# Kernel optimization log

Hardware: AMD Instinct MI355X
Metric: run time of the kernel (lower is better)

The kernel has to match this reference:

```python
import jax, jax.numpy as jnp
import numpy as np

B, N, D = 16, 1369, 1024
HID, NH = 512, 8
SCALE = np.sqrt(D // NH)


def _pos_encoding_2d(n, d):
    ps = int(np.sqrt(n))  # 37; n is a perfect square here
    div = jnp.exp(jnp.arange(0, d // 2, 2, dtype=jnp.float32) * (-np.log(10000.0) / (d // 2)))
    rows = (jnp.arange(n) // ps).astype(jnp.float32)
    cols = (jnp.arange(n) % ps).astype(jnp.float32)
    def interleave(s, c):
        return jnp.stack([s, c], axis=-1).reshape(n, -1)
    half_row = interleave(jnp.sin(rows[:, None] * div), jnp.cos(rows[:, None] * div))
    half_col = interleave(jnp.sin(cols[:, None] * div), jnp.cos(cols[:, None] * div))
    return jnp.concatenate([half_row, half_col], axis=-1)  # [n, d]


def _center_bias(n, strength=0.3):
    ps = int(np.sqrt(n))
    c = ps // 2
    y, x = jnp.meshgrid(jnp.arange(ps, dtype=jnp.float32), jnp.arange(ps, dtype=jnp.float32), indexing='ij')
    d2 = (x - c) ** 2 + (y - c) ** 2
    sigma = ps / 6.0
    return (jnp.exp(-d2 / (2.0 * sigma ** 2)).reshape(-1)) * strength  # [n]


def setup_inputs() -> dict:
    key = jax.random.key(0)
    ks = jax.random.split(key, 16)
    s = 0.02
    return {
        'patch_tokens': jax.random.normal(ks[0], (B, N, D), dtype=jnp.float32),
        'curiosity_score': jax.random.uniform(ks[1], (B,), dtype=jnp.float32),
        'Wq': jax.random.normal(ks[2], (D, D), dtype=jnp.float32) * s,
        'bq': jax.random.uniform(ks[3], (D,), minval=-0.05, maxval=0.05, dtype=jnp.float32),
        'Wk': jax.random.normal(ks[4], (D, D), dtype=jnp.float32) * s,
        'bk': jax.random.uniform(ks[5], (D,), minval=-0.05, maxval=0.05, dtype=jnp.float32),
        'Wv': jax.random.normal(ks[6], (D, D), dtype=jnp.float32) * s,
        'bv': jnp.zeros((D,), dtype=jnp.float32),
        'Wc1': jax.random.normal(ks[7], (1, HID // 8), dtype=jnp.float32) * s,
        'bc1': jnp.zeros((HID // 8,), dtype=jnp.float32),
        'Wc2': jax.random.normal(ks[8], (HID // 8, NH), dtype=jnp.float32) * s,
        'bc2': jnp.zeros((NH,), dtype=jnp.float32),
        'Wp1': jax.random.normal(ks[9], (D, HID), dtype=jnp.float32) * s,
        'bp1': jnp.zeros((HID,), dtype=jnp.float32),
        'Wp2': jax.random.normal(ks[10], (HID, HID // 4), dtype=jnp.float32) * s,
        'bp2': jnp.zeros((HID // 4,), dtype=jnp.float32),
        'adaptive_weight': jnp.float32(0.5),
    }


def reference(patch_tokens, curiosity_score, Wq, bq, Wk, bk, Wv, bv,
              Wc1, bc1, Wc2, bc2, Wp1, bp1, Wp2, bp2, adaptive_weight):
    b, n, d = patch_tokens.shape
    x = patch_tokens + _pos_encoding_2d(n, d)[None]  # [B,N,D]

    q = x @ Wq + bq
    k = x @ Wk + bk
    v = x @ Wv + bv

    scores = jnp.einsum('bqd,bkd->bqk', q, k) / SCALE          # [B,N,N]
    attn = jax.nn.softmax(scores, axis=-1)                     # dropout p=0 / eval
    attended = jnp.einsum('bqk,bkd->bqd', attn, v)             # [B,N,D]

    cb = _center_bias(n)[None]                                 # [1,N]
    VAR_EPS = 1e-6

    pa = attn.mean(axis=1) + cb
    # fallback chain (data-dependent in torch; expressed with jnp.where)
    pa2 = jnp.diagonal(attn, axis1=-2, axis2=-1) + cb
    pa = jnp.where(jnp.var(pa, ddof=1) < VAR_EPS, pa2, pa)
    pa3 = attn.max(axis=-1) + cb
    pa = jnp.where(jnp.var(pa, ddof=1) < VAR_EPS, pa3, pa)
    norms = jnp.linalg.norm(x, axis=-1)
    noise = jax.random.normal(jax.random.key(42), norms.shape, dtype=norms.dtype) * 0.1 * jnp.std(norms, ddof=1)
    pa = jnp.where(jnp.var(pa, ddof=1) < VAR_EPS, norms + noise, pa)

    pa = pa / (pa.sum(axis=-1, keepdims=True) + 1e-8)

    # curiosity modulation
    h = jax.nn.relu(curiosity_score[:, None] @ Wc1 + bc1)
    cm = jax.nn.sigmoid(h @ Wc2 + bc2)                         # [B,NH]
    cw = cm.mean(axis=-1, keepdims=True)                       # [B,1]
    modulated = pa * (1.0 + cw)
    fa = adaptive_weight * modulated + (1.0 - adaptive_weight) * pa

    fa = jnp.clip(fa, 1e-8, None)
    fa = fa / (fa.sum(axis=-1, keepdims=True) + 1e-8)

    weighted = jnp.sum(attended * fa[..., None], axis=1)       # [B,D]
    focal = jax.nn.relu(weighted @ Wp1 + bp1) @ Wp2 + bp2      # [B,HID//4]
    return focal, fa
```

## Files before the change

kernel.cpp:

```cpp
#include <hip/hip_runtime.h>
#include <hip/hip_bf16.h>
#include <cstdint>

#define B_   16
#define N_   1369
#define NP   1536
#define D_   1024
#define NQKV 3072

typedef __bf16 bf16x8_t __attribute__((ext_vector_type(8)));
typedef __bf16 bf16x4_t __attribute__((ext_vector_type(4)));
typedef float  f32x4_t  __attribute__((ext_vector_type(4)));

__device__ __forceinline__ float  bf2f(__bf16 x) { return (float)x; }
__device__ __forceinline__ __bf16 f2bf(float x)  { return (__bf16)x; }

#define GLOAD_LDS16(g, l) __builtin_amdgcn_global_load_lds( \
    (const __attribute__((address_space(1))) void*)(g),     \
    (__attribute__((address_space(3))) void*)(l), 16, 0, 0)

__global__ __launch_bounds__(256)
void pos_kernel(float* __restrict__ pos)
{
    const int idx = blockIdx.x * 256 + threadIdx.x;
    if (idx >= N_ * D_) return;
    const int n = idx >> 10, f = idx & 1023;
    const int row = n / 37, col = n - row * 37;
    const float base = (f < 512) ? (float)row : (float)col;
    const int  t2   = (f & 511) >> 1;
    const float dv  = __expf(-0.03597789207803197f * (float)t2);
    const float ang = base * dv;
    pos[idx] = (f & 1) ? cosf(ang) : sinf(ang);
}

__global__ __launch_bounds__(256)
void addpos_kernel(const float* __restrict__ patch, const float* __restrict__ pos,
                   __bf16* __restrict__ X)
{
    const long tid = (long)blockIdx.x * 256 + threadIdx.x;
    const long e   = tid * 4;
    const int  f   = (int)(e & 1023);
    const long nb  = e >> 10;
    const int  n   = (int)(nb % NP);
    const long b   = nb / NP;
    bf16x4_t o;
    if (n < N_) {
        const float4 p = *(const float4*)(patch + ((b * N_ + n) << 10) + f);
        const float4 q = *(const float4*)(pos + ((long)n << 10) + f);
        o[0] = f2bf(p.x + q.x); o[1] = f2bf(p.y + q.y);
        o[2] = f2bf(p.z + q.z); o[3] = f2bf(p.w + q.w);
    } else {
        o[0] = o[1] = o[2] = o[3] = f2bf(0.f);
    }
    *(bf16x4_t*)(X + e) = o;
}

__global__ __launch_bounds__(256)
void wcast_kernel(const float* __restrict__ W0, const float* __restrict__ W1,
                  const float* __restrict__ W2,
                  __bf16* __restrict__ T0, __bf16* __restrict__ T1, __bf16* __restrict__ T2)
{
    const float* W = blockIdx.z == 0 ? W0 : (blockIdx.z == 1 ? W1 : W2);
    __bf16*      T = blockIdx.z == 0 ? T0 : (blockIdx.z == 1 ? T1 : T2);
    __shared__ float tile[64][65];
    const int o0 = blockIdx.x * 64, i0 = blockIdx.y * 64;
    const int t = threadIdx.x;
    const int tr = t >> 4, tc = (t & 15) * 4;
    #pragma unroll
    for (int rr = 0; rr < 64; rr += 16) {
        float4 v = *(const float4*)(W + (long)(i0 + rr + tr) * 1024 + o0 + tc);
        tile[rr + tr][tc + 0] = v.x; tile[rr + tr][tc + 1] = v.y;
        tile[rr + tr][tc + 2] = v.z; tile[rr + tr][tc + 3] = v.w;
    }
    __syncthreads();
    #pragma unroll
    for (int rr = 0; rr < 64; rr += 16) {
        bf16x4_t o;
        o[0] = f2bf(tile[tc + 0][rr + tr]); o[1] = f2bf(tile[tc + 1][rr + tr]);
        o[2] = f2bf(tile[tc + 2][rr + tr]); o[3] = f2bf(tile[tc + 3][rr + tr]);
        *(bf16x4_t*)(T + (long)(o0 + rr + tr) * 1024 + i0 + tc) = o;
    }
}

__global__ __launch_bounds__(256)
void bcat_kernel(const float* __restrict__ bq, const float* __restrict__ bk,
                 const float* __restrict__ bv, float* __restrict__ bcat)
{
    const int i = blockIdx.x * 256 + threadIdx.x;
    if (i >= NQKV) return;
    const int p = i >> 10, j = i & 1023;
    bcat[i] = p == 0 ? bq[j] : (p == 1 ? bk[j] : bv[j]);
}

template<int HAS_BIAS>
__global__ __launch_bounds__(512, 2)
void gemm256(const __bf16* __restrict__ A, const __bf16* __restrict__ Bt,
             __bf16* __restrict__ C, const float* __restrict__ bias,
             int lda, int ldb, int ldc, int Kd, float scale,
             long sA, long sB, long sC, int tilesN, int tilesPerBatch, int cpx)
{
    __shared__ __bf16 lds[65536];
    const int bid = blockIdx.x;
    const int vt  = (bid & 7) * cpx + (bid >> 3);
    const int bz  = vt / tilesPerBatch;
    const int rem = vt - bz * tilesPerBatch;
    const int ty  = rem / tilesN;
    const int tx  = rem - ty * tilesN;
    A  += (long)bz * sA;  Bt += (long)bz * sB;  C += (long)bz * sC;
    const int m0 = ty * 256, n0 = tx * 256;

    const int t  = threadIdx.x;
    const int w  = t >> 6, l = t & 63;
    const int wr = w >> 2, wc = w & 3;
    const int lr = l & 15, lh = l >> 4;

    const int laneF  = (lr * 64 + ((lh * 16) ^ (((lr >> 3) & 1) << 5))) >> 1;
    const int rstage = w * 16 + (l >> 2);
    const int kstage = ((l & 3) * 8) ^ (((l >> 5) & 1) << 4);

    const __bf16* Ag = A  + (long)(m0 + rstage) * lda + kstage;
    const __bf16* Bg = Bt + (long)(n0 + rstage) * ldb + kstage;
    __bf16* dA = lds + (w * 2) * 512;
    __bf16* dB = lds + 16384 + (w * 2) * 512;

#define SA_(buf, half, kt) do {                                       \
    const __bf16* g_ = Ag + (long)(half) * 128 * lda + (kt) * 64;     \
    __bf16* d_ = dA + (buf) * 32768 + (half) * 8192;                  \
    GLOAD_LDS16(g_, d_); GLOAD_LDS16(g_ + 32, d_ + 512); } while (0)
#define SB_(buf, half, kt) do {                                       \
    const __bf16* g_ = Bg + (long)(half) * 128 * ldb + (kt) * 64;     \
    __bf16* d_ = dB + (buf) * 32768 + (half) * 8192;                  \
    GLOAD_LDS16(g_, d_); GLOAD_LDS16(g_ + 32, d_ + 512); } while (0)

    f32x4_t acc[8][4] = {};
    bf16x8_t bfr[4][2];

#define BREADS_() do { const __bf16* bp_ = lds + cbB + laneF;                              \
    bfr[0][0] = *(const bf16x8_t*)(bp_);        bfr[0][1] = *(const bf16x8_t*)(bp_ + 512); \
    bfr[1][0] = *(const bf16x8_t*)(bp_ + 1024); bfr[1][1] = *(const bf16x8_t*)(bp_ + 1536);\
    bfr[2][0] = *(const bf16x8_t*)(bp_ + 2048); bfr[2][1] = *(const bf16x8_t*)(bp_ + 2560);\
    bfr[3][0] = *(const bf16x8_t*)(bp_ + 3072); bfr[3][1] = *(const bf16x8_t*)(bp_ + 3584);} while (0)

#define PHASE_(p, P0R, STG, VMW) do {                                                  \
    const __bf16* ap_ = lds + cbase + wr * 8192 + (p) * 2048 + laneF;                  \
    bf16x8_t a00 = *(const bf16x8_t*)(ap_);                                            \
    bf16x8_t a01 = *(const bf16x8_t*)(ap_ + 512);                                      \
    bf16x8_t a10 = *(const bf16x8_t*)(ap_ + 1024);                                     \
    bf16x8_t a11 = *(const bf16x8_t*)(ap_ + 1536);                                     \
    P0R;                                                                               \
    STG;                                                                               \
    __builtin_amdgcn_s_barrier();                                                      \
    asm volatile("s_waitcnt lgkmcnt(0)" ::: "memory");                                 \
    __builtin_amdgcn_sched_barrier(0);                                                 \
    __builtin_amdgcn_s_setprio(1);                                                     \
    _Pragma("unroll") for (int nn = 0; nn < 4; ++nn)                                   \
      acc[(p)*2+0][nn] = __builtin_amdgcn_mfma_f32_16x16x32_bf16(a00, bfr[nn][0], acc[(p)*2+0][nn], 0, 0, 0); \
    _Pragma("unroll") for (int nn = 0; nn < 4; ++nn)                                   \
      acc[(p)*2+1][nn] = __builtin_amdgcn_mfma_f32_16x16x32_bf16(a10, bfr[nn][0], acc[(p)*2+1][nn], 0, 0, 0); \
    _Pragma("unroll") for (int nn = 0; nn < 4; ++nn)                                   \
      acc[(p)*2+0][nn] = __builtin_amdgcn_mfma_f32_16x16x32_bf16(a01, bfr[nn][1], acc[(p)*2+0][nn], 0, 0, 0); \
    _Pragma("unroll") for (int nn = 0; nn < 4; ++nn)                                   \
      acc[(p)*2+1][nn] = __builtin_amdgcn_mfma_f32_16x16x32_bf16(a11, bfr[nn][1], acc[(p)*2+1][nn], 0, 0, 0); \
    __builtin_amdgcn_s_setprio(0);                                                     \
    VMW;                                                                               \
    __builtin_amdgcn_s_barrier();                                                      \
  } while (0)

    const int NT = Kd >> 6;
    SA_(0, 0, 0); SA_(0, 1, 0); SB_(0, 0, 0); SB_(0, 1, 0);
    SB_(1, 0, 1); SB_(1, 1, 1);
    asm volatile("s_waitcnt vmcnt(4)" ::: "memory");
    __builtin_amdgcn_s_barrier();

    for (int tk = 0; tk < NT; ++tk) {
        const int c  = tk & 1, o = c ^ 1;
        const int t1 = (tk + 1 < NT) ? tk + 1 : NT - 1;
        const int t2 = (tk + 2 < NT) ? tk + 2 : NT - 1;
        const int cbase = c * 32768;
        const int cbB   = cbase + 16384 + wc * 4096;
        PHASE_(0, BREADS_(), SA_(o, 0, t1), ((void)0));
        PHASE_(1, ((void)0), SA_(o, 1, t1), ((void)0));
        PHASE_(2, ((void)0), SB_(c, 0, t2), ((void)0));
        PHASE_(3, ((void)0), SB_(c, 1, t2),
               asm volatile("s_waitcnt vmcnt(4)" ::: "memory"));
    }

    #pragma unroll
    for (int mi = 0; mi < 8; ++mi) {
        const int row = m0 + wr * 128 + mi * 16 + lh * 4;
        #pragma unroll
        for (int nn = 0; nn < 4; ++nn) {
            const int col = n0 + wc * 64 + nn * 16 + lr;
            const float bb = HAS_BIAS ? bias[col] : 0.0f;
            #pragma unroll
            for (int q = 0; q < 4; ++q)
                C[(long)(row + q) * ldc + col] = f2bf(acc[mi][nn][q] * scale + bb);
        }
    }
#undef SA_
#undef SB_
#undef BREADS_
#undef PHASE_
}

__global__ __launch_bounds__(256)
void softmax_kernel(__bf16* __restrict__ S)
{
    const int q = blockIdx.x, b = blockIdx.y;
    __bf16* row = S + ((long)b * NP + q) * NP;
    const int t = threadIdx.x;
    float v[6];
    float m = -1e30f;
    #pragma unroll
    for (int i = 0; i < 6; ++i) {
        const int k = t + i * 256;
        float x = -1e30f;
        if (k < N_) x = bf2f(row[k]);
        v[i] = x;
        m = fmaxf(m, x);
    }
    __shared__ float red[8];
    #pragma unroll
    for (int o = 32; o; o >>= 1) m = fmaxf(m, __shfl_xor(m, o));
    if (!(t & 63)) red[t >> 6] = m;
    __syncthreads();
    m = fmaxf(fmaxf(red[0], red[1]), fmaxf(red[2], red[3]));
    float s = 0.f;
    #pragma unroll
    for (int i = 0; i < 6; ++i) {
        const int k = t + i * 256;
        if (k < N_) { const float e = __expf(v[i] - m); v[i] = e; s += e; }
    }
    #pragma unroll
    for (int o = 32; o; o >>= 1) s += __shfl_xor(s, o);
    if (!(t & 63)) red[4 + (t >> 6)] = s;
    __syncthreads();
    s = red[4] + red[5] + red[6] + red[7];
    const float inv = 1.f / s;
    #pragma unroll
    for (int i = 0; i < 6; ++i) {
        const int k = t + i * 256;
        if (k < N_)      row[k] = f2bf(v[i] * inv);
        else             row[k] = f2bf(0.f);
    }
}

template<int WEIGHTED>
__global__ __launch_bounds__(256)
void colsum_kernel(const __bf16* __restrict__ attn, const float* __restrict__ wv,
                   float* __restrict__ out)
{
    const int k = blockIdx.x * 256 + threadIdx.x;
    const int b = blockIdx.y;
    const int q0 = blockIdx.z * 172;
    const int q1 = (q0 + 172 < N_) ? q0 + 172 : N_;
    if (k >= N_) return;
    const __bf16* base = attn + (long)b * NP * NP + k;
    float s = 0.f;
    for (int q = q0; q < q1; ++q) {
        float a = bf2f(base[(long)q * NP]);
        if (WEIGHTED) a *= wv[b * NP + q];
        s += a;
    }
    atomicAdd(out + b * NP + k, s);
}

__global__ __launch_bounds__(256)
void fa_kernel(const float* __restrict__ pa_raw, const float* __restrict__ curiosity,
               const float* __restrict__ Wc1, const float* __restrict__ bc1,
               const float* __restrict__ Wc2, const float* __restrict__ bc2,
               const float* __restrict__ aw_p,
               float* __restrict__ fa_ws, float* __restrict__ out_fa)
{
    const int b = blockIdx.x, t = threadIdx.x;
    __shared__ float hsh[64];
    __shared__ float red[8];
    __shared__ float cwsh;
    if (t < 64) hsh[t] = fmaxf(0.f, curiosity[b] * Wc1[t] + bc1[t]);
    __syncthreads();
    if (t < 8) {
        float a = bc2[t];
        for (int j = 0; j < 64; ++j) a += hsh[j] * Wc2[j * 8 + t];
        red[t] = 1.f / (1.f + __expf(-a));
    }
    __syncthreads();
    if (t == 0) {
        float cw = 0.f;
        for (int i = 0; i < 8; ++i) cw += red[i];
        cwsh = cw * 0.125f;
    }
    __syncthreads();
    const float aw   = aw_p[0];
    const float modf = 1.f + aw * cwsh;
    const float sig  = 37.f / 6.f;
    const float inv2s2 = 1.f / (2.f * sig * sig);
    float pv[6];
    float s1 = 0.f;
    #pragma unroll
    for (int i = 0; i < 6; ++i) {
        const int k = t + i * 256;
        float p = 0.f;
        if (k < N_) {
            const int y = k / 37, x = k - y * 37;
            const float d2 = (float)((x - 18) * (x - 18) + (y - 18) * (y - 18));
            const float cb = 0.3f * __expf(-d2 * inv2s2);
            p = pa_raw[b * NP + k] * (1.f / 1369.f) + cb;
        }
        pv[i] = p; s1 += p;
    }
    #pragma unroll
    for (int o = 32; o; o >>= 1) s1 += __shfl_xor(s1, o);
    __syncthreads();
    if (!(t & 63)) red[t >> 6] = s1;
    __syncthreads();
    s1 = red[0] + red[1] + red[2] + red[3];
    const float inv1 = 1.f / (s1 + 1e-8f);
    float s2 = 0.f;
    #pragma unroll
    for (int i = 0; i < 6; ++i) {
        const int k = t + i * 256;
        if (k < N_) {
            const float f = fmaxf(pv[i] * inv1 * modf, 1e-8f);
            pv[i] = f; s2 += f;
        }
    }
    #pragma unroll
    for (int o = 32; o; o >>= 1) s2 += __shfl_xor(s2, o);
    if (!(t & 63)) red[4 + (t >> 6)] = s2;
    __syncthreads();
    s2 = red[4] + red[5] + red[6] + red[7];
    const float inv2 = 1.f / (s2 + 1e-8f);
    #pragma unroll
    for (int i = 0; i < 6; ++i) {
        const int k = t + i * 256;
        if (k < N_) {
            const float f = pv[i] * inv2;
            fa_ws[b * NP + k]  = f;
            out_fa[b * N_ + k] = f;
        }
    }
}

__global__ __launch_bounds__(256)
void weighted_kernel(const float* __restrict__ g, const __bf16* __restrict__ V,
                     int ldv, float* __restrict__ wout)
{
    const int b  = blockIdx.y;
    const int k0 = blockIdx.x * 86;
    const int k1 = (k0 + 86 < N_) ? k0 + 86 : N_;
    const int d  = threadIdx.x * 4;
    float a0 = 0, a1 = 0, a2 = 0, a3 = 0;
    const __bf16* vb = V + (long)b * NP * ldv + d;
    for (int k = k0; k < k1; ++k) {
        const float gv = g[b * NP + k];
        bf16x4_t vv = *(const bf16x4_t*)(vb + (long)k * ldv);
        a0 += gv * bf2f(vv[0]); a1 += gv * bf2f(vv[1]);
        a2 += gv * bf2f(vv[2]); a3 += gv * bf2f(vv[3]);
    }
    atomicAdd(wout + b * D_ + d + 0, a0);
    atomicAdd(wout + b * D_ + d + 1, a1);
    atomicAdd(wout + b * D_ + d + 2, a2);
    atomicAdd(wout + b * D_ + d + 3, a3);
}

__global__ __launch_bounds__(256)
void focal_kernel(const float* __restrict__ weighted, const float* __restrict__ Wp1,
                  const float* __restrict__ bp1, const float* __restrict__ Wp2,
                  const float* __restrict__ bp2, float* __restrict__ out)
{
    const int b = blockIdx.x, t = threadIdx.x;
    __shared__ float wsh[1024];
    __shared__ float hsh[512];
    for (int i = t; i < 1024; i += 256) wsh[i] = weighted[b * 1024 + i];
    __syncthreads();
    for (int j = t; j < 512; j += 256) {
        float a = bp1[j];
        for (int d2 = 0; d2 < 1024; ++d2) a += wsh[d2] * Wp1[d2 * 512 + j];
        hsh[j] = fmaxf(a, 0.f);
    }
    __syncthreads();
    for (int o = t; o < 128; o += 256) {
        float a = bp2[o];
        for (int j = 0; j < 512; ++j) a += hsh[j] * Wp2[j * 128 + o];
        out[b * 128 + o] = a;
    }
}

extern "C" void kernel_launch(void* const* d_in, const int* in_sizes, int n_in,
                              void* d_out, int out_size, void* d_ws, size_t ws_size,
                              hipStream_t stream)
{
    const float* patch     = (const float*)d_in[0];
    const float* curiosity = (const float*)d_in[1];
    const float* Wq  = (const float*)d_in[2];
    const float* bq  = (const float*)d_in[3];
    const float* Wk  = (const float*)d_in[4];
    const float* bk  = (const float*)d_in[5];
    const float* Wv  = (const float*)d_in[6];
    const float* bv  = (const float*)d_in[7];
    const float* Wc1 = (const float*)d_in[8];
    const float* bc1 = (const float*)d_in[9];
    const float* Wc2 = (const float*)d_in[10];
    const float* bc2 = (const float*)d_in[11];
    const float* Wp1 = (const float*)d_in[12];
    const float* bp1 = (const float*)d_in[13];
    const float* Wp2 = (const float*)d_in[14];
    const float* bp2 = (const float*)d_in[15];
    const float* aw  = (const float*)d_in[16];
    float* out = (float*)d_out;

    char* ws = (char*)d_ws;
    size_t off = 0;
    auto alloc = [&](size_t bytes) -> char* {
        char* p = ws + off;
        off += (bytes + 255) & ~(size_t)255;
        return p;
    };
    float*  pos  = (float*) alloc((size_t)N_ * D_ * 4);
    __bf16* X    = (__bf16*)alloc((size_t)B_ * NP * D_ * 2);
    __bf16* WT   = (__bf16*)alloc((size_t)3 * D_ * D_ * 2);
    const size_t S_BYTES = (size_t)B_ * NP * NP * 2;
    if (off < S_BYTES) off = S_BYTES;
    __bf16* S    = (__bf16*)ws;
    __bf16* QKV  = (__bf16*)alloc((size_t)B_ * NP * NQKV * 2);
    float*  pa   = (float*) alloc((size_t)B_ * NP * 4);
    float*  faw  = (float*) alloc((size_t)B_ * NP * 4);
    float*  gbuf = (float*) alloc((size_t)B_ * NP * 4);
    float*  wsum = (float*) alloc((size_t)B_ * D_ * 4);
    float*  bcat = (float*) alloc((size_t)NQKV * 4);

    (void)hipMemsetAsync(pa,   0, (size_t)B_ * NP * 4, stream);
    (void)hipMemsetAsync(gbuf, 0, (size_t)B_ * NP * 4, stream);
    (void)hipMemsetAsync(wsum, 0, (size_t)B_ * D_ * 4, stream);

    pos_kernel<<<(N_ * D_ + 255) / 256, 256, 0, stream>>>(pos);
    addpos_kernel<<<(int)((size_t)B_ * NP * D_ / 4 / 256), 256, 0, stream>>>(patch, pos, X);
    {
        dim3 g(16, 16, 3);
        wcast_kernel<<<g, 256, 0, stream>>>(Wq, Wk, Wv,
                                            WT, WT + D_ * D_, WT + 2 * D_ * D_);
    }
    bcat_kernel<<<(NQKV + 255) / 256, 256, 0, stream>>>(bq, bk, bv, bcat);
    {
        const int nwg = 96 * 12;
        gemm256<1><<<nwg, 512, 0, stream>>>(X, WT, QKV, bcat,
                                            D_, D_, NQKV, D_, 1.0f,
                                            0, 0, 0, 12, nwg, nwg / 8);
    }
    {
        const int nwg = 36 * B_;
        gemm256<0><<<nwg, 512, 0, stream>>>(QKV, QKV + D_, S, nullptr,
                                            NQKV, NQKV, NP, D_,
                                            0.08838834764831845f,
                                            (long)NP * NQKV, (long)NP * NQKV,
                                            (long)NP * NP, 6, 36, nwg / 8);
    }
    {
        dim3 g(N_, B_);
        softmax_kernel<<<g, 256, 0, stream>>>(S);
    }
    {
        dim3 g(6, B_, 8);
        colsum_kernel<0><<<g, 256, 0, stream>>>(S, nullptr, pa);
    }
    fa_kernel<<<B_, 256, 0, stream>>>(pa, curiosity, Wc1, bc1, Wc2, bc2, aw,
                                      faw, out + B_ * 128);
    {
        dim3 g(6, B_, 8);
        colsum_kernel<1><<<g, 256, 0, stream>>>(S, faw, gbuf);
    }
    {
        dim3 g(16, B_);
        weighted_kernel<<<g, 256, 0, stream>>>(gbuf, QKV + 2 * D_, NQKV, wsum);
    }
    focal_kernel<<<B_, 256, 0, stream>>>(wsum, Wp1, bp1, Wp2, bp2, out);
}
```

Measured before the change: 537.0 us.

## Pad S and QKV row strides, vectorize softmax and column-sum kernels

Pads the score matrix row stride to 1568 and the QKV row stride to 3104 so that rows no longer land on power-of-two strides. This is meant to reduce channel or bank conflicts in the GEMM epilogues and in the strided reads. Softmax is rewritten as one wave per row with 16-byte vector loads and stores, and LDS reductions are replaced by shuffles. The column-sum kernels now read 8-wide vectors over 16-row chunks, which issues more atomics in exchange for coalesced loads. The padding also enlarges the workspace.

```diff
diff --git a/kernel.cpp b/kernel.cpp
--- a/kernel.cpp
+++ b/kernel.cpp
@@ -7,6 +7,8 @@
 #define NP   1536
 #define D_   1024
 #define NQKV 3072
+#define SLD  1568
+#define QLD  3104
 
 typedef __bf16 bf16x8_t __attribute__((ext_vector_type(8)));
 typedef __bf16 bf16x4_t __attribute__((ext_vector_type(4)));
@@ -206,42 +208,46 @@
 __global__ __launch_bounds__(256)
 void softmax_kernel(__bf16* __restrict__ S)
 {
-    const int q = blockIdx.x, b = blockIdx.y;
-    __bf16* row = S + ((long)b * NP + q) * NP;
-    const int t = threadIdx.x;
-    float v[6];
+    const int wid  = threadIdx.x >> 6;
+    const int lane = threadIdx.x & 63;
+    const int q    = blockIdx.x * 4 + wid;
+    const int b    = blockIdx.y;
+    if (q >= N_) return;
+    __bf16* row = S + ((long)b * NP + q) * SLD;
+    float v[24];
     float m = -1e30f;
     #pragma unroll
-    for (int i = 0; i < 6; ++i) {
-        const int k = t + i * 256;
-        float x = -1e30f;
-        if (k < N_) x = bf2f(row[k]);
-        v[i] = x;
-        m = fmaxf(m, x);
-    }
-    __shared__ float red[8];
+    for (int j = 0; j < 3; ++j) {
+        const int k0 = j * 512 + lane * 8;
+        bf16x8_t raw = *(const bf16x8_t*)(row + k0);
+        #pragma unroll
+        for (int i = 0; i < 8; ++i) {
+            const float x = (k0 + i < N_) ? bf2f(raw[i]) : -1e30f;
+            v[j * 8 + i] = x; m = fmaxf(m, x);
+        }
+    }
     #pragma unroll
     for (int o = 32; o; o >>= 1) m = fmaxf(m, __shfl_xor(m, o));
-    if (!(t & 63)) red[t >> 6] = m;
-    __syncthreads();
-    m = fmaxf(fmaxf(red[0], red[1]), fmaxf(red[2], red[3]));
     float s = 0.f;
     #pragma unroll
-    for (int i = 0; i < 6; ++i) {
-        const int k = t + i * 256;
-        if (k < N_) { const float e = __expf(v[i] - m); v[i] = e; s += e; }
+    for (int j = 0; j < 3; ++j) {
+        const int k0 = j * 512 + lane * 8;
+        #pragma unroll
+        for (int i = 0; i < 8; ++i) {
+            if (k0 + i < N_) { const float e = __expf(v[j * 8 + i] - m); v[j * 8 + i] = e; s += e; }
+            else             v[j * 8 + i] = 0.f;
+        }
     }
     #pragma unroll
     for (int o = 32; o; o >>= 1) s += __shfl_xor(s, o);
-    if (!(t & 63)) red[4 + (t >> 6)] = s;
-    __syncthreads();
-    s = red[4] + red[5] + red[6] + red[7];
     const float inv = 1.f / s;
     #pragma unroll
-    for (int i = 0; i < 6; ++i) {
-        const int k = t + i * 256;
-        if (k < N_)      row[k] = f2bf(v[i] * inv);
-        else             row[k] = f2bf(0.f);
+    for (int j = 0; j < 3; ++j) {
+        const int k0 = j * 512 + lane * 8;
+        bf16x8_t o8;
+        #pragma unroll
+        for (int i = 0; i < 8; ++i) o8[i] = f2bf(v[j * 8 + i] * inv);
+        *(bf16x8_t*)(row + k0) = o8;
     }
 }
 
@@ -250,19 +256,22 @@
 void colsum_kernel(const __bf16* __restrict__ attn, const float* __restrict__ wv,
                    float* __restrict__ out)
 {
-    const int k = blockIdx.x * 256 + threadIdx.x;
-    const int b = blockIdx.y;
-    const int q0 = blockIdx.z * 172;
-    const int q1 = (q0 + 172 < N_) ? q0 + 172 : N_;
-    if (k >= N_) return;
-    const __bf16* base = attn + (long)b * NP * NP + k;
-    float s = 0.f;
+    const int t = threadIdx.x;
+    if (t >= 192) return;
+    const int b  = blockIdx.y;
+    const int q0 = blockIdx.x * 16;
+    const int q1 = (q0 + 16 < N_) ? q0 + 16 : N_;
+    const int k8 = t * 8;
+    float s[8] = {};
+    const __bf16* base = attn + (long)b * NP * SLD + k8;
     for (int q = q0; q < q1; ++q) {
-        float a = bf2f(base[(long)q * NP]);
-        if (WEIGHTED) a *= wv[b * NP + q];
-        s += a;
-    }
-    atomicAdd(out + b * NP + k, s);
+        bf16x8_t v = *(const bf16x8_t*)(base + (long)q * SLD);
+        const float wq = WEIGHTED ? wv[b * NP + q] : 1.0f;
+        #pragma unroll
+        for (int i = 0; i < 8; ++i) s[i] += wq * bf2f(v[i]);
+    }
+    #pragma unroll
+    for (int i = 0; i < 8; ++i) atomicAdd(out + b * NP + k8 + i, s[i]);
 }
 
 __global__ __launch_bounds__(256)
@@ -419,10 +428,10 @@
     float*  pos  = (float*) alloc((size_t)N_ * D_ * 4);
     __bf16* X    = (__bf16*)alloc((size_t)B_ * NP * D_ * 2);
     __bf16* WT   = (__bf16*)alloc((size_t)3 * D_ * D_ * 2);
-    const size_t S_BYTES = (size_t)B_ * NP * NP * 2;
+    const size_t S_BYTES = (size_t)B_ * NP * SLD * 2;
     if (off < S_BYTES) off = S_BYTES;
     __bf16* S    = (__bf16*)ws;
-    __bf16* QKV  = (__bf16*)alloc((size_t)B_ * NP * NQKV * 2);
+    __bf16* QKV  = (__bf16*)alloc((size_t)B_ * NP * QLD * 2);
     float*  pa   = (float*) alloc((size_t)B_ * NP * 4);
     float*  faw  = (float*) alloc((size_t)B_ * NP * 4);
     float*  gbuf = (float*) alloc((size_t)B_ * NP * 4);
@@ -444,34 +453,34 @@
     {
         const int nwg = 96 * 12;
         gemm256<1><<<nwg, 512, 0, stream>>>(X, WT, QKV, bcat,
-                                            D_, D_, NQKV, D_, 1.0f,
+                                            D_, D_, QLD, D_, 1.0f,
                                             0, 0, 0, 12, nwg, nwg / 8);
     }
     {
         const int nwg = 36 * B_;
         gemm256<0><<<nwg, 512, 0, stream>>>(QKV, QKV + D_, S, nullptr,
-                                            NQKV, NQKV, NP, D_,
+                                            QLD, QLD, SLD, D_,
                                             0.08838834764831845f,
-                                            (long)NP * NQKV, (long)NP * NQKV,
-                                            (long)NP * NP, 6, 36, nwg / 8);
-    }
-    {
-        dim3 g(N_, B_);
+                                            (long)NP * QLD, (long)NP * QLD,
+                                            (long)NP * SLD, 6, 36, nwg / 8);
+    }
+    {
+        dim3 g((N_ + 3) / 4, B_);
         softmax_kernel<<<g, 256, 0, stream>>>(S);
     }
     {
-        dim3 g(6, B_, 8);
+        dim3 g(86, B_);
         colsum_kernel<0><<<g, 256, 0, stream>>>(S, nullptr, pa);
     }
     fa_kernel<<<B_, 256, 0, stream>>>(pa, curiosity, Wc1, bc1, Wc2, bc2, aw,
                                       faw, out + B_ * 128);
     {
-        dim3 g(6, B_, 8);
+        dim3 g(86, B_);
         colsum_kernel<1><<<g, 256, 0, stream>>>(S, faw, gbuf);
     }
     {
         dim3 g(16, B_);
-        weighted_kernel<<<g, 256, 0, stream>>>(gbuf, QKV + 2 * D_, NQKV, wsum);
+        weighted_kernel<<<g, 256, 0, stream>>>(gbuf, QKV + 2 * D_, QLD, wsum);
     }
     focal_kernel<<<B_, 256, 0, stream>>>(wsum, Wp1, bp1, Wp2, bp2, out);
 }
```

After: 599.5 us. 11.6% more time.
